# Optimization experiments

Hardware: AMD Instinct MI355X
Metric: run time of the kernel (lower is better)

Reference implementation:

```python
import jax, jax.numpy as jnp
import numpy as np

B, K, C, H, W = 16, 32, 256, 80, 80
NH, HD = 8, 32          # num_heads, head_dim (C = NH*HD)
S = 4                   # fixed roi_align sampling grid per 1x1 output bin
EPS = 1e-5


def _bn(x, g, b, m, v):
    # inference-mode BatchNorm2d, NCHW
    s = g / jnp.sqrt(v + EPS)
    return x * s[None, :, None, None] + (b - m * s)[None, :, None, None]


def _bilinear(feat, ys, xs):
    # feat [B,C,H,W]; ys,xs [B,K,S,S] -> [B,K,S,S,C], torchvision roi_align semantics
    Hh, Ww = feat.shape[2], feat.shape[3]
    valid = (ys >= -1.0) & (ys <= Hh) & (xs >= -1.0) & (xs <= Ww)
    y = jnp.clip(ys, 0.0, Hh - 1.0)
    x = jnp.clip(xs, 0.0, Ww - 1.0)
    y0 = jnp.floor(y); x0 = jnp.floor(x)
    y0i = y0.astype(jnp.int32); x0i = x0.astype(jnp.int32)
    y1i = jnp.minimum(y0i + 1, Hh - 1); x1i = jnp.minimum(x0i + 1, Ww - 1)
    ly = y - y0; lx = x - x0; hy = 1.0 - ly; hx = 1.0 - lx
    bidx = jnp.arange(feat.shape[0])[:, None, None, None]
    g = lambda yi, xi: feat[bidx, :, yi, xi]  # -> [B,K,S,S,C]
    val = ((hy * hx)[..., None] * g(y0i, x0i) + (hy * lx)[..., None] * g(y0i, x1i)
           + (ly * hx)[..., None] * g(y1i, x0i) + (ly * lx)[..., None] * g(y1i, x1i))
    return val * valid[..., None].astype(val.dtype)


def _roi_align_1x1(feat, boxes):
    # boxes [B,K,4] normalized xyxy; spatial_scale = 1.0 in the source
    Hh, Ww = feat.shape[2], feat.shape[3]
    sc = jnp.asarray([Ww - 1, Hh - 1, Ww - 1, Hh - 1], feat.dtype)
    ab = boxes * sc
    x1, y1, x2, y2 = ab[..., 0], ab[..., 1], ab[..., 2], ab[..., 3]
    rw = jnp.maximum(x2 - x1, 1.0)
    rh = jnp.maximum(y2 - y1, 1.0)
    grid = (jnp.arange(S, dtype=feat.dtype) + 0.5) / S
    ys = y1[..., None] + grid * rh[..., None]   # [B,K,S]
    xs = x1[..., None] + grid * rw[..., None]
    ys2, xs2 = jnp.broadcast_arrays(ys[..., :, None], xs[..., None, :])  # [B,K,S,S]
    vals = _bilinear(feat, ys2, xs2)            # [B,K,S,S,C]
    return vals.mean(axis=(2, 3)).reshape(feat.shape[0] * boxes.shape[1], -1)


def _gat(nodes, wq, bq, wk, bkp, wv, bv, scale, wo, bo, ln_g, ln_b):
    Bk = nodes.shape[0]
    q = (nodes @ wq.T + bq).reshape(Bk, NH, HD)
    k = (nodes @ wk.T + bkp).reshape(Bk, NH, HD)
    v = (nodes @ wv.T + bv).reshape(Bk, NH, HD)
    scores = jnp.einsum('ihd,jhd->ijh', q, k) * scale
    attn = jax.nn.softmax(scores, axis=1)       # softmax over keys j
    msg = jnp.einsum('ijh,jhd->ihd', attn, v).reshape(Bk, NH * HD)
    y = nodes + msg @ wo.T + bo
    mu = y.mean(-1, keepdims=True)
    var = ((y - mu) ** 2).mean(-1, keepdims=True)
    return (y - mu) / jnp.sqrt(var + EPS) * ln_g + ln_b


def _forward(x, boxes, conv_w, conv_b, bn1_g, bn1_b, bn1_m, bn1_v,
             wq, bq, wk, bkp, wv, bv, scale, wo, bo, ln_g, ln_b,
             rec_w, rec_b, bn2_g, bn2_b, bn2_m, bn2_v):
    feat = jax.lax.conv_general_dilated(
        x, conv_w, (1, 1), 'SAME',
        dimension_numbers=('NCHW', 'OIHW', 'NCHW')) + conv_b[None, :, None, None]
    feat = _bn(feat, bn1_g, bn1_b, bn1_m, bn1_v)
    feat = feat * jax.nn.sigmoid(feat)          # SiLU
    nodes = _roi_align_1x1(feat, boxes)         # [B*K, C]
    enh = _gat(nodes, wq, bq, wk, bkp, wv, bv, scale, wo, bo, ln_g, ln_b)
    f = enh.reshape(B, K, C)
    wts = jax.nn.softmax(f.mean(-1), axis=1)    # [B,K]
    weighted = jnp.einsum('bkc,bk->bc', f, wts)
    # out map is spatially constant -> 1x1 conv + BN collapse to per-sample affine
    y = weighted @ rec_w[:, :, 0, 0].T + rec_b
    s = bn2_g / jnp.sqrt(bn2_v + EPS)
    y = y * s + (bn2_b - bn2_m * s)
    return x + y[:, :, None, None]


def setup_inputs() -> dict:
    key = jax.random.key(0)
    ks = jax.random.split(key, 10)
    x = jax.random.normal(ks[0], (B, C, H, W), jnp.float32)
    bx = jax.random.uniform(ks[1], (B, K, 4), jnp.float32)
    bx = bx.at[:, :, 2:].add(bx[:, :, :2])      # xy2 += xy1
    boxes = jnp.clip(bx, 0.0, 1.0)
    w = lambda k, shp: jax.random.normal(k, shp, jnp.float32) * 0.02
    return {
        'x': x, 'boxes': boxes,
        'conv_w': w(ks[2], (C, C, 3, 3)), 'conv_b': jnp.zeros((C,), jnp.float32),
        'bn1_g': jnp.ones((C,), jnp.float32), 'bn1_b': jnp.zeros((C,), jnp.float32),
        'bn1_m': jnp.zeros((C,), jnp.float32), 'bn1_v': jnp.ones((C,), jnp.float32),
        'wq': w(ks[3], (C, C)), 'bq': jnp.zeros((C,), jnp.float32),
        'wk': w(ks[4], (C, C)), 'bkp': jnp.zeros((C,), jnp.float32),
        'wv': w(ks[5], (C, C)), 'bv': jnp.zeros((C,), jnp.float32),
        'scale': jnp.asarray(1.0 / np.sqrt(HD), jnp.float32),
        'wo': w(ks[6], (C, C)), 'bo': jnp.zeros((C,), jnp.float32),
        'ln_g': jnp.ones((C,), jnp.float32), 'ln_b': jnp.zeros((C,), jnp.float32),
        'rec_w': w(ks[7], (C, C, 1, 1)), 'rec_b': jnp.zeros((C,), jnp.float32),
        'bn2_g': jnp.ones((C,), jnp.float32), 'bn2_b': jnp.zeros((C,), jnp.float32),
        'bn2_m': jnp.zeros((C,), jnp.float32), 'bn2_v': jnp.ones((C,), jnp.float32),
    }


def reference(x, boxes, conv_w, conv_b, bn1_g, bn1_b, bn1_m, bn1_v,
              wq, bq, wk, bkp, wv, bv, scale, wo, bo, ln_g, ln_b,
              rec_w, rec_b, bn2_g, bn2_b, bn2_m, bn2_v):
    return _forward(x, boxes, conv_w, conv_b, bn1_g, bn1_b, bn1_m, bn1_v,
                    wq, bq, wk, bkp, wv, bv, scale, wo, bo, ln_g, ln_b,
                    rec_w, rec_b, bn2_g, bn2_b, bn2_m, bn2_v)
```

## Files before the change

### kernel.cpp

```cpp
#include <hip/hip_runtime.h>

#define EPSV 1e-5f

typedef __attribute__((ext_vector_type(8))) short short8v;
typedef __attribute__((ext_vector_type(4))) float f32x4;

static __device__ __forceinline__ unsigned short f2bf(float f) {
  unsigned int u = __float_as_uint(f);
  u += 0x7fff + ((u >> 16) & 1);
  return (unsigned short)(u >> 16);
}
static __device__ __forceinline__ float bf2f(unsigned short h) {
  return __uint_as_float(((unsigned int)h) << 16);
}

static __device__ __forceinline__ void glds16(const void* g, void* l) {
  __builtin_amdgcn_global_load_lds(
      (const __attribute__((address_space(1))) void*)g,
      (__attribute__((address_space(3))) void*)l, 16, 0, 0);
}

__global__ __launch_bounds__(256) void prep_fused_kernel(
    const float* __restrict__ x, unsigned short* __restrict__ xin,
    const float* __restrict__ cw, unsigned short* __restrict__ Wr,
    float* __restrict__ zpad,
    const float* __restrict__ wq, const float* __restrict__ wk,
    const float* __restrict__ wv, const float* __restrict__ wo,
    const float* __restrict__ rec, float* __restrict__ wT)
{
  __shared__ unsigned short t[80 * 257];
  const int bid = blockIdx.x;
  if (bid < 1280) {
    int b = bid / 80, y = bid - b * 80;
    const float* src = x + (size_t)b * 256 * 6400 + y * 80;
    for (int e = threadIdx.x; e < 256 * 20; e += 256) {
      int c = e / 20;
      int px4 = e - c * 20;
      f32x4 v = *(const f32x4*)&src[(size_t)c * 6400 + px4 * 4];
#pragma unroll
      for (int j = 0; j < 4; ++j)
        t[(px4 * 4 + j) * 257 + c] = f2bf(v[j]);
    }
    __syncthreads();
    unsigned short* dst = xin + (size_t)bid * 80 * 256;
    for (int e = threadIdx.x; e < 80 * 32; e += 256) {
      int px = e >> 5;
      int c8 = e & 31;
      short8v v;
#pragma unroll
      for (int j = 0; j < 8; ++j) v[j] = t[px * 257 + c8 * 8 + j];
      *(short8v*)&dst[px * 256 + c8 * 8] = v;
    }
  } else if (bid < 3584) {
    if (bid == 1280) zpad[threadIdx.x] = 0.f;
    int idx = (bid - 1280) * 256 + threadIdx.x;
    int cil = idx & 31;
    int rest = idx >> 5;
    int co = rest & 255;
    int tcc = rest >> 8;
    int cc = tcc & 7;
    int tt = tcc >> 3;
    int dy = tt / 3, dx = tt - dy * 3;
    int ci = cc * 32 + cil;
    Wr[idx] = f2bf(cw[((co * 256 + ci) * 3 + dy) * 3 + dx]);
  } else {
    int idx = (bid - 3584) * 256 + threadIdx.x;
    int m = idx >> 16;
    int e = idx & 65535;
    int ci = e >> 8, co = e & 255;
    const float* src = (m == 0) ? wq : (m == 1) ? wk : (m == 2) ? wv
                     : (m == 3) ? wo : rec;
    wT[idx] = src[co * 256 + ci];
  }
}

__global__ __launch_bounds__(512, 1) void roiconv_kernel(
    const unsigned short* __restrict__ xin,
    const float* __restrict__ boxes,
    const float* __restrict__ convb,
    const float* __restrict__ bn1g, const float* __restrict__ bn1b,
    const float* __restrict__ bn1m, const float* __restrict__ bn1v,
    const unsigned short* __restrict__ Wr,
    float* __restrict__ nodes)
{
  const int bid = blockIdx.x;
  const int pr = (bid & 7) * 32 + (bid >> 3);
  const int tid = threadIdx.x;
  const int nd = tid >> 8;
  const int n = pr * 2 + nd;
  const int b = n >> 5;
  const int w = tid >> 6, lane = tid & 63;
  const int bq = lane >> 4, r16 = lane & 15;
  const int wr = w >> 2, wc = w & 3;

  __shared__ __align__(16) char lds[74240];
  float* wcoef = (float*)(lds + 73728);
  const int INB = 0, WB = 24576;

  const int pc = (tid >> 2) & 63;
  const float* bx = boxes + n * 4;
  float x1 = bx[0] * 79.f, y1 = bx[1] * 79.f, x2 = bx[2] * 79.f, y2 = bx[3] * 79.f;
  float rwd = fmaxf(x2 - x1, 1.f), rh = fmaxf(y2 - y1, 1.f);
  int s = pc >> 2;
  int sy = s >> 2, sx = s & 3;
  float yy = y1 + (sy + 0.5f) * 0.25f * rh;
  float xx = x1 + (sx + 0.5f) * 0.25f * rwd;
  bool valid = (yy >= -1.f) && (yy <= 80.f) && (xx >= -1.f) && (xx <= 80.f);
  float yc = fminf(fmaxf(yy, 0.f), 79.f), xc = fminf(fmaxf(xx, 0.f), 79.f);
  float y0f = floorf(yc), x0f = floorf(xc);
  int y0i = (int)y0f, x0i = (int)x0f;
  int y1i = min(y0i + 1, 79), x1i = min(x0i + 1, 79);
  float ly = yc - y0f, lx = xc - x0f, hy = 1.f - ly, hx = 1.f - lx;
  int py = (pc & 2) ? y1i : y0i;
  int pxx = (pc & 1) ? x1i : x0i;
  if ((tid & 3) == 0)
    wcoef[tid >> 2] = ((pc & 2) ? ly : hy) * ((pc & 1) ? lx : hx) *
                      (valid ? 0.0625f : 0.f);

  const int chunk = (tid & 3) ^ ((pc >> 1) & 3);
  unsigned ioff[9];
#pragma unroll
  for (int t = 0; t < 9; ++t) {
    int dy = t / 3, dx = t - dy * 3;
    int cy = py + dy - 1, cx = pxx + dx - 1;
    bool ok = ((unsigned)cy < 80u) && ((unsigned)cx < 80u);
    ioff[t] = ok ? (unsigned)((((b * 80 + cy) * 80 + cx) * 256 + chunk * 8) * 2)
                 : 52428800u;
  }
  unsigned woff[2];
#pragma unroll
  for (int i = 0; i < 2; ++i) {
    int s2 = tid + (i << 9);
    int wco = s2 >> 2;
    int wch = (s2 & 3) ^ ((wco >> 1) & 3);
    woff[i] = (unsigned)((wco * 32 + wch * 8) * 2);
  }
  const int laneoff = r16 * 64 + ((bq ^ ((r16 >> 1) & 3)) << 4);
  const char* xinb = (const char*)xin;
  const char* Wrb = (const char*)Wr;
  const int ldwave = w << 10;

  f32x4 acc[4][4];
#pragma unroll
  for (int i = 0; i < 4; ++i)
#pragma unroll
    for (int j = 0; j < 4; ++j)
      acc[i][j] = (f32x4){0.f, 0.f, 0.f, 0.f};

  glds16(xinb + ioff[0], lds + INB + ldwave);
  glds16(Wrb + woff[0], lds + WB + ldwave);
  glds16(Wrb + woff[1], lds + WB + 8192 + ldwave);
  glds16(xinb + ioff[1], lds + INB + 8192 + ldwave);
  glds16(Wrb + ((size_t)8 << 14) + woff[0], lds + WB + 16384 + ldwave);
  glds16(Wrb + ((size_t)8 << 14) + woff[1], lds + WB + 16384 + 8192 + ldwave);

  for (int cc = 0; cc < 8; ++cc) {
#pragma unroll
    for (int t = 0; t < 9; ++t) {
      const int cb = t % 3;
      const char* inb = lds + INB + cb * 8192;
      const char* wb  = lds + WB + cb * 16384;
      if (cc == 7 && t == 8)
        asm volatile("s_waitcnt vmcnt(0)" ::: "memory");
      else
        asm volatile("s_waitcnt vmcnt(3)" ::: "memory");
      __builtin_amdgcn_s_barrier();
      __builtin_amdgcn_sched_barrier(0);
      if (!(cc == 7 && t >= 7)) {
        const int nt = (t + 2 > 8) ? t - 7 : t + 2;
        const int nb = nt % 3;
        const int ncc = cc + (t >= 7 ? 1 : 0);
        char* innx = lds + INB + nb * 8192;
        char* wbn  = lds + WB + nb * 16384;
        glds16(xinb + ioff[nt] + ncc * 64, innx + ldwave);
        const char* wg = Wrb + ((size_t)(nt * 8 + ncc) << 14);
        glds16(wg + woff[0], wbn + ldwave);
        glds16(wg + woff[1], wbn + 8192 + ldwave);
      }
      const char* pa = inb + wr * 4096 + laneoff;
      const char* pw = wb + wc * 4096 + laneoff;
      short8v af0 = *(const short8v*)(pa);
      short8v af1 = *(const short8v*)(pa + 1024);
      short8v af2 = *(const short8v*)(pa + 2048);
      short8v af3 = *(const short8v*)(pa + 3072);
      short8v wf0 = *(const short8v*)(pw);
      short8v wf1 = *(const short8v*)(pw + 1024);
      short8v wf2 = *(const short8v*)(pw + 2048);
      short8v wf3 = *(const short8v*)(pw + 3072);
      __builtin_amdgcn_s_setprio(1);
      acc[0][0] = __builtin_amdgcn_mfma_f32_16x16x32_bf16(af0, wf0, acc[0][0], 0, 0, 0);
      acc[0][1] = __builtin_amdgcn_mfma_f32_16x16x32_bf16(af0, wf1, acc[0][1], 0, 0, 0);
      acc[0][2] = __builtin_amdgcn_mfma_f32_16x16x32_bf16(af0, wf2, acc[0][2], 0, 0, 0);
      acc[0][3] = __builtin_amdgcn_mfma_f32_16x16x32_bf16(af0, wf3, acc[0][3], 0, 0, 0);
      acc[1][0] = __builtin_amdgcn_mfma_f32_16x16x32_bf16(af1, wf0, acc[1][0], 0, 0, 0);
      acc[1][1] = __builtin_amdgcn_mfma_f32_16x16x32_bf16(af1, wf1, acc[1][1], 0, 0, 0);
      acc[1][2] = __builtin_amdgcn_mfma_f32_16x16x32_bf16(af1, wf2, acc[1][2], 0, 0, 0);
      acc[1][3] = __builtin_amdgcn_mfma_f32_16x16x32_bf16(af1, wf3, acc[1][3], 0, 0, 0);
      acc[2][0] = __builtin_amdgcn_mfma_f32_16x16x32_bf16(af2, wf0, acc[2][0], 0, 0, 0);
      acc[2][1] = __builtin_amdgcn_mfma_f32_16x16x32_bf16(af2, wf1, acc[2][1], 0, 0, 0);
      acc[2][2] = __builtin_amdgcn_mfma_f32_16x16x32_bf16(af2, wf2, acc[2][2], 0, 0, 0);
      acc[2][3] = __builtin_amdgcn_mfma_f32_16x16x32_bf16(af2, wf3, acc[2][3], 0, 0, 0);
      acc[3][0] = __builtin_amdgcn_mfma_f32_16x16x32_bf16(af3, wf0, acc[3][0], 0, 0, 0);
      acc[3][1] = __builtin_amdgcn_mfma_f32_16x16x32_bf16(af3, wf1, acc[3][1], 0, 0, 0);
      acc[3][2] = __builtin_amdgcn_mfma_f32_16x16x32_bf16(af3, wf2, acc[3][2], 0, 0, 0);
      acc[3][3] = __builtin_amdgcn_mfma_f32_16x16x32_bf16(af3, wf3, acc[3][3], 0, 0, 0);
      __builtin_amdgcn_s_setprio(0);
    }
  }
  __syncthreads();

  unsigned short* ep = (unsigned short*)lds;
#pragma unroll
  for (int cf = 0; cf < 4; ++cf) {
    int co = wc * 64 + cf * 16 + r16;
    float sc = bn1g[co] / sqrtf(bn1v[co] + EPSV);
    float sh = bn1b[co] - bn1m[co] * sc;
    float cb = convb[co];
#pragma unroll
    for (int mf = 0; mf < 4; ++mf) {
#pragma unroll
      for (int rg = 0; rg < 4; ++rg) {
        int pxo = wr * 64 + mf * 16 + bq * 4 + rg;
        float v = (acc[mf][cf][rg] + cb) * sc + sh;
        v = v / (1.f + __expf(-v));
        ep[pxo * 264 + co] = f2bf(v);
      }
    }
  }
  __syncthreads();
  const int c = tid & 255;
  float val = 0.f;
#pragma unroll
  for (int p = 0; p < 64; ++p)
    val += wcoef[nd * 64 + p] * bf2f(ep[(nd * 64 + p) * 264 + c]);
  nodes[n * 256 + c] = val;
}

__global__ __launch_bounds__(256) void qkv_kernel(
    const float* __restrict__ nodes, const float* __restrict__ wT,
    const float* __restrict__ bq, const float* __restrict__ bk,
    const float* __restrict__ bv,
    float* __restrict__ q, float* __restrict__ k, float* __restrict__ v)
{
  const int blk = blockIdx.x;
  const int co = threadIdx.x;
  __shared__ float nd[4][256];
  for (int i = threadIdx.x; i < 1024; i += 256)
    nd[i >> 8][i & 255] = nodes[blk * 1024 + i];
  __syncthreads();
  float aq[4] = {0, 0, 0, 0};
  float ak[4] = {0, 0, 0, 0};
  float av[4] = {0, 0, 0, 0};
  const float* wqT = wT;
  const float* wkT = wT + 65536;
  const float* wvT = wT + 131072;
  for (int ci = 0; ci < 256; ++ci) {
    float wq_ = wqT[ci * 256 + co];
    float wk_ = wkT[ci * 256 + co];
    float wv_ = wvT[ci * 256 + co];
#pragma unroll
    for (int r = 0; r < 4; ++r) {
      float nv = nd[r][ci];
      aq[r] += nv * wq_;
      ak[r] += nv * wk_;
      av[r] += nv * wv_;
    }
  }
  float bq_ = bq[co], bk_ = bk[co], bv_ = bv[co];
#pragma unroll
  for (int r = 0; r < 4; ++r) {
    int n = blk * 4 + r;
    q[n * 256 + co] = aq[r] + bq_;
    k[n * 256 + co] = ak[r] + bk_;
    v[n * 256 + co] = av[r] + bv_;
  }
}

__global__ __launch_bounds__(256) void attn_mh_kernel(
    const float* __restrict__ q, const float* __restrict__ k,
    const float* __restrict__ v, const float* __restrict__ scale_p,
    float* __restrict__ msgs)
{
  const int bid = blockIdx.x;
  const int h = bid & 7, qc = bid >> 3;
  const int q0 = qc * 16;
  const int tid = threadIdx.x;
  __shared__ __align__(16) float Kh[512 * 32];
  __shared__ __align__(16) float Vh[512 * 32];
  __shared__ unsigned short pb[16 * 512];

  for (int idx = tid; idx < 4096; idx += 256) {
    int j = idx >> 3, part = idx & 7;
    int chs = part ^ (j & 7);
    *(f32x4*)&Kh[j * 32 + chs * 4] =
        *(const f32x4*)&k[(size_t)j * 256 + h * 32 + part * 4];
    *(f32x4*)&Vh[j * 32 + chs * 4] =
        *(const f32x4*)&v[(size_t)j * 256 + h * 32 + part * 4];
  }
  const int qi = tid >> 4, l = tid & 15;
  f32x4 qr[8];
#pragma unroll
  for (int p = 0; p < 8; ++p)
    qr[p] = *(const f32x4*)&q[(size_t)(q0 + qi) * 256 + h * 32 + p * 4];
  const float scale = scale_p[0];
  __syncthreads();

  float pj[32];
  float mx = -1e30f;
#pragma unroll
  for (int jj = 0; jj < 32; ++jj) {
    int j = jj * 16 + l;
    const float* kr = &Kh[j * 32];
    int sw = j & 7;
    float s = 0.f;
#pragma unroll
    for (int p = 0; p < 8; ++p) {
      f32x4 kv = *(const f32x4*)&kr[(p ^ sw) * 4];
      s += kv.x * qr[p].x + kv.y * qr[p].y + kv.z * qr[p].z + kv.w * qr[p].w;
    }
    s *= scale;
    pj[jj] = s;
    mx = fmaxf(mx, s);
  }
#pragma unroll
  for (int o = 1; o < 16; o <<= 1) mx = fmaxf(mx, __shfl_xor(mx, o, 16));
  float sum = 0.f;
#pragma unroll
  for (int jj = 0; jj < 32; ++jj) {
    float e = __expf(pj[jj] - mx);
    pj[jj] = e;
    sum += e;
  }
#pragma unroll
  for (int o = 1; o < 16; o <<= 1) sum += __shfl_xor(sum, o, 16);
  float inv = 1.f / sum;
#pragma unroll
  for (int jj = 0; jj < 32; ++jj)
    pb[qi * 512 + jj * 16 + l] = f2bf(pj[jj] * inv);
  __syncthreads();

  float m0 = 0.f, m1 = 0.f;
  const unsigned short* pq = &pb[qi * 512];
  for (int j = 0; j < 512; ++j) {
    float p = bf2f(pq[j]);
    int chs = (l >> 1) ^ (j & 7);
    const float* vr = &Vh[j * 32 + chs * 4 + ((2 * l) & 3)];
    m0 += p * vr[0];
    m1 += p * vr[1];
  }
  float* mo = &msgs[(size_t)(q0 + qi) * 256 + h * 32 + 2 * l];
  mo[0] = m0;
  mo[1] = m1;
}

__global__ __launch_bounds__(256) void outln_kernel(
    const float* __restrict__ msgs, const float* __restrict__ nodes,
    const float* __restrict__ woT, const float* __restrict__ bo,
    const float* __restrict__ lng, const float* __restrict__ lnb,
    float* __restrict__ enh)
{
  const int blk = blockIdx.x;
  const int co = threadIdx.x;
  __shared__ float ms[8][256];
  __shared__ float red1[8][4], red2[8][4];
  for (int i = co; i < 2048; i += 256)
    ms[i >> 8][i & 255] = msgs[blk * 2048 + i];
  __syncthreads();
  float yv[8];
  float bo_ = bo[co];
#pragma unroll
  for (int r = 0; r < 8; ++r)
    yv[r] = nodes[(size_t)(blk * 8 + r) * 256 + co] + bo_;
  for (int ci = 0; ci < 256; ++ci) {
    float w = woT[ci * 256 + co];
#pragma unroll
    for (int r = 0; r < 8; ++r) yv[r] += ms[r][ci] * w;
  }
  const int wv = co >> 6, lane = co & 63;
#pragma unroll
  for (int r = 0; r < 8; ++r) {
    float s1 = yv[r], s2 = yv[r] * yv[r];
#pragma unroll
    for (int o = 1; o < 64; o <<= 1) {
      s1 += __shfl_xor(s1, o);
      s2 += __shfl_xor(s2, o);
    }
    if (lane == 0) { red1[r][wv] = s1; red2[r][wv] = s2; }
  }
  __syncthreads();
  float lg = lng[co], lb = lnb[co];
#pragma unroll
  for (int r = 0; r < 8; ++r) {
    float S1 = red1[r][0] + red1[r][1] + red1[r][2] + red1[r][3];
    float S2 = red2[r][0] + red2[r][1] + red2[r][2] + red2[r][3];
    float mu = S1 * (1.f / 256.f);
    float var = S2 * (1.f / 256.f) - mu * mu;
    enh[(size_t)(blk * 8 + r) * 256 + co] =
        (yv[r] - mu) * rsqrtf(var + EPSV) * lg + lb;
  }
}

__global__ __launch_bounds__(256) void final_kernel(
    const float* __restrict__ enh, const float* __restrict__ recT,
    const float* __restrict__ recb,
    const float* __restrict__ bn2g, const float* __restrict__ bn2b,
    const float* __restrict__ bn2m, const float* __restrict__ bn2v,
    float* __restrict__ yfin)
{
  const int b = blockIdx.x;
  const int tid = threadIdx.x;
  const int wv = tid >> 6, l = tid & 63;
  __shared__ float rm[32], wts[32], wgt[256];
  for (int kk = wv; kk < 32; kk += 4) {
    const float* er = enh + (size_t)(b * 32 + kk) * 256;
    float s = er[l] + er[l + 64] + er[l + 128] + er[l + 192];
#pragma unroll
    for (int o = 1; o < 64; o <<= 1) s += __shfl_xor(s, o);
    if (l == 0) rm[kk] = s * (1.f / 256.f);
  }
  __syncthreads();
  if (tid < 32) {
    float m = rm[tid];
    float mx = m;
#pragma unroll
    for (int o = 1; o < 32; o <<= 1) mx = fmaxf(mx, __shfl_xor(mx, o, 32));
    float e = __expf(m - mx);
    float sm = e;
#pragma unroll
    for (int o = 1; o < 32; o <<= 1) sm += __shfl_xor(sm, o, 32);
    wts[tid] = e / sm;
  }
  __syncthreads();
  float wsum = 0.f;
  for (int kk = 0; kk < 32; ++kk)
    wsum += enh[(size_t)(b * 32 + kk) * 256 + tid] * wts[kk];
  wgt[tid] = wsum;
  __syncthreads();
  const int co = tid;
  float yv = recb[co];
  for (int ci = 0; ci < 256; ++ci)
    yv += wgt[ci] * recT[ci * 256 + co];
  float s = bn2g[co] / sqrtf(bn2v[co] + EPSV);
  yfin[b * 256 + co] = yv * s + (bn2b[co] - bn2m[co] * s);
}

__global__ __launch_bounds__(256) void add_kernel(
    const float* __restrict__ x, const float* __restrict__ yfin,
    float* __restrict__ out)
{
  const int bc = blockIdx.x;
  const float a = yfin[bc];
  const f32x4* xp = (const f32x4*)(x + (size_t)bc * 6400);
  f32x4* op = (f32x4*)(out + (size_t)bc * 6400);
  for (int i = threadIdx.x; i < 1600; i += 256) {
    f32x4 v = xp[i];
    v.x += a; v.y += a; v.z += a; v.w += a;
    op[i] = v;
  }
}

extern "C" void kernel_launch(void* const* d_in, const int* in_sizes, int n_in,
                              void* d_out, int out_size, void* d_ws, size_t ws_size,
                              hipStream_t stream)
{
  const float* x      = (const float*)d_in[0];
  const float* boxes  = (const float*)d_in[1];
  const float* conv_w = (const float*)d_in[2];
  const float* conv_b = (const float*)d_in[3];
  const float* bn1g   = (const float*)d_in[4];
  const float* bn1b   = (const float*)d_in[5];
  const float* bn1m   = (const float*)d_in[6];
  const float* bn1v   = (const float*)d_in[7];
  const float* wq     = (const float*)d_in[8];
  const float* bq     = (const float*)d_in[9];
  const float* wk     = (const float*)d_in[10];
  const float* bkp    = (const float*)d_in[11];
  const float* wv     = (const float*)d_in[12];
  const float* bv     = (const float*)d_in[13];
  const float* scale  = (const float*)d_in[14];
  const float* wo     = (const float*)d_in[15];
  const float* bo     = (const float*)d_in[16];
  const float* lng    = (const float*)d_in[17];
  const float* lnb    = (const float*)d_in[18];
  const float* rec_w  = (const float*)d_in[19];
  const float* rec_b  = (const float*)d_in[20];
  const float* bn2g   = (const float*)d_in[21];
  const float* bn2b   = (const float*)d_in[22];
  const float* bn2m   = (const float*)d_in[23];
  const float* bn2v   = (const float*)d_in[24];
  float* out = (float*)d_out;

  char* ws = (char*)d_ws;
  unsigned short* Wr = (unsigned short*)(ws);
  float* wT    = (float*)(ws + 53608448);
  float* nodes = (float*)(ws + 54919168);
  float* qb    = nodes + 131072;
  float* kb    = qb + 131072;
  float* vb    = kb + 131072;
  float* enh   = vb + 131072;
  float* yfin  = enh + 131072;
  float* msgs  = yfin + 4096;

  unsigned short* xin = (unsigned short*)d_out;
  float* zpad = (float*)((char*)d_out + 52428800);

  hipLaunchKernelGGL(prep_fused_kernel, dim3(4864), dim3(256), 0, stream,
                     x, xin, conv_w, Wr, zpad, wq, wk, wv, wo, rec_w, wT);
  hipLaunchKernelGGL(roiconv_kernel, dim3(256), dim3(512), 0, stream,
                     xin, boxes, conv_b, bn1g, bn1b, bn1m, bn1v, Wr, nodes);
  hipLaunchKernelGGL(qkv_kernel, dim3(128), dim3(256), 0, stream,
                     nodes, wT, bq, bkp, bv, qb, kb, vb);
  hipLaunchKernelGGL(attn_mh_kernel, dim3(256), dim3(256), 0, stream,
                     qb, kb, vb, scale, msgs);
  hipLaunchKernelGGL(outln_kernel, dim3(64), dim3(256), 0, stream,
                     msgs, nodes, wT + 3 * 65536, bo, lng, lnb, enh);
  hipLaunchKernelGGL(final_kernel, dim3(16), dim3(256), 0, stream,
                     enh, wT + 4 * 65536, rec_b, bn2g, bn2b, bn2m, bn2v, yfin);
  hipLaunchKernelGGL(add_kernel, dim3(4096), dim3(256), 0, stream, x, yfin, out);
}
```

Baseline: 182.2 us.

## Split roiconv output channels across blocks and add residual from bf16 NHWC copy

The ROI conv kernel moves from 256 blocks of 512 threads to 512 blocks of 256 threads. Each block now handles both nodes of a pair but only half of the 256 output channels. This halves LDS per block and allows two blocks per CU, at the cost of loading the gathered input twice. The final residual add now reads the bf16 NHWC copy of x held in workspace instead of the fp32 input, and transposes it through LDS back to NCHW. That halves the residual read traffic but adds bf16 rounding error to the output.

New measurement: 187.6 us. +2.9%, slower.

```diff
diff --git a/kernel.cpp b/kernel.cpp
--- a/kernel.cpp
+++ b/kernel.cpp
@@ -74,7 +74,7 @@
   }
 }
 
-__global__ __launch_bounds__(512, 1) void roiconv_kernel(
+__global__ __launch_bounds__(256, 2) void roiconv_kernel(
     const unsigned short* __restrict__ xin,
     const float* __restrict__ boxes,
     const float* __restrict__ convb,
@@ -84,61 +84,65 @@
     float* __restrict__ nodes)
 {
   const int bid = blockIdx.x;
-  const int pr = (bid & 7) * 32 + (bid >> 3);
+  const int blk = (bid & 7) * 64 + (bid >> 3);
+  const int pr = blk >> 1, coh = blk & 1;
   const int tid = threadIdx.x;
-  const int nd = tid >> 8;
-  const int n = pr * 2 + nd;
-  const int b = n >> 5;
   const int w = tid >> 6, lane = tid & 63;
   const int bq = lane >> 4, r16 = lane & 15;
-  const int wr = w >> 2, wc = w & 3;
-
-  __shared__ __align__(16) char lds[74240];
-  float* wcoef = (float*)(lds + 73728);
+  const int wr = w >> 1, wc = w & 1;
+
+  __shared__ __align__(16) char lds[49664];
+  float* wcoef = (float*)(lds + 49152);
   const int INB = 0, WB = 24576;
 
-  const int pc = (tid >> 2) & 63;
-  const float* bx = boxes + n * 4;
-  float x1 = bx[0] * 79.f, y1 = bx[1] * 79.f, x2 = bx[2] * 79.f, y2 = bx[3] * 79.f;
-  float rwd = fmaxf(x2 - x1, 1.f), rh = fmaxf(y2 - y1, 1.f);
-  int s = pc >> 2;
-  int sy = s >> 2, sx = s & 3;
-  float yy = y1 + (sy + 0.5f) * 0.25f * rh;
-  float xx = x1 + (sx + 0.5f) * 0.25f * rwd;
-  bool valid = (yy >= -1.f) && (yy <= 80.f) && (xx >= -1.f) && (xx <= 80.f);
-  float yc = fminf(fmaxf(yy, 0.f), 79.f), xc = fminf(fmaxf(xx, 0.f), 79.f);
-  float y0f = floorf(yc), x0f = floorf(xc);
-  int y0i = (int)y0f, x0i = (int)x0f;
-  int y1i = min(y0i + 1, 79), x1i = min(x0i + 1, 79);
-  float ly = yc - y0f, lx = xc - x0f, hy = 1.f - ly, hx = 1.f - lx;
-  int py = (pc & 2) ? y1i : y0i;
-  int pxx = (pc & 1) ? x1i : x0i;
-  if ((tid & 3) == 0)
-    wcoef[tid >> 2] = ((pc & 2) ? ly : hy) * ((pc & 1) ? lx : hx) *
-                      (valid ? 0.0625f : 0.f);
-
-  const int chunk = (tid & 3) ^ ((pc >> 1) & 3);
-  unsigned ioff[9];
-#pragma unroll
-  for (int t = 0; t < 9; ++t) {
-    int dy = t / 3, dx = t - dy * 3;
-    int cy = py + dy - 1, cx = pxx + dx - 1;
-    bool ok = ((unsigned)cy < 80u) && ((unsigned)cx < 80u);
-    ioff[t] = ok ? (unsigned)((((b * 80 + cy) * 80 + cx) * 256 + chunk * 8) * 2)
-                 : 52428800u;
-  }
-  unsigned woff[2];
-#pragma unroll
-  for (int i = 0; i < 2; ++i) {
-    int s2 = tid + (i << 9);
-    int wco = s2 >> 2;
-    int wch = (s2 & 3) ^ ((wco >> 1) & 3);
-    woff[i] = (unsigned)((wco * 32 + wch * 8) * 2);
-  }
+  const int pc = tid >> 2;
+  const int swz = tid & 3;
+  const int chunk = swz ^ ((pc >> 1) & 3);
+  unsigned ioff[2][9];
+#pragma unroll
+  for (int nd2 = 0; nd2 < 2; ++nd2) {
+    const int n2 = pr * 2 + nd2;
+    const int b2 = n2 >> 5;
+    const float* bx = boxes + n2 * 4;
+    float x1 = bx[0] * 79.f, y1 = bx[1] * 79.f;
+    float x2 = bx[2] * 79.f, y2 = bx[3] * 79.f;
+    float rwd = fmaxf(x2 - x1, 1.f), rh = fmaxf(y2 - y1, 1.f);
+    int s = pc >> 2;
+    int sy = s >> 2, sx = s & 3;
+    float yy = y1 + (sy + 0.5f) * 0.25f * rh;
+    float xx = x1 + (sx + 0.5f) * 0.25f * rwd;
+    bool valid = (yy >= -1.f) && (yy <= 80.f) && (xx >= -1.f) && (xx <= 80.f);
+    float yc = fminf(fmaxf(yy, 0.f), 79.f), xc = fminf(fmaxf(xx, 0.f), 79.f);
+    float y0f = floorf(yc), x0f = floorf(xc);
+    int y0i = (int)y0f, x0i = (int)x0f;
+    int y1i = min(y0i + 1, 79), x1i = min(x0i + 1, 79);
+    float ly = yc - y0f, lx = xc - x0f, hy = 1.f - ly, hx = 1.f - lx;
+    int py = (pc & 2) ? y1i : y0i;
+    int pxx = (pc & 1) ? x1i : x0i;
+    if (swz == 0)
+      wcoef[nd2 * 64 + pc] = ((pc & 2) ? ly : hy) * ((pc & 1) ? lx : hx) *
+                             (valid ? 0.0625f : 0.f);
+#pragma unroll
+    for (int t = 0; t < 9; ++t) {
+      int dy = t / 3, dx = t - dy * 3;
+      int cy = py + dy - 1, cx = pxx + dx - 1;
+      bool ok = ((unsigned)cy < 80u) && ((unsigned)cx < 80u);
+      ioff[nd2][t] = ok
+          ? (unsigned)((((b2 * 80 + cy) * 80 + cx) * 256 + chunk * 8) * 2)
+          : 52428800u;
+    }
+  }
+  const int wco0 = tid >> 2;
+  const unsigned woff0 =
+      (unsigned)(coh * 8192 + (wco0 * 32 + ((swz ^ ((wco0 >> 1) & 3)) * 8)) * 2);
+  const int wco1 = 64 + wco0;
+  const unsigned woff1 =
+      (unsigned)(coh * 8192 + (wco1 * 32 + ((swz ^ ((wco1 >> 1) & 3)) * 8)) * 2);
+
   const int laneoff = r16 * 64 + ((bq ^ ((r16 >> 1) & 3)) << 4);
   const char* xinb = (const char*)xin;
   const char* Wrb = (const char*)Wr;
-  const int ldwave = w << 10;
+  const int ldwave = (w << 6) << 4;
 
   f32x4 acc[4][4];
 #pragma unroll
@@ -147,23 +151,25 @@
     for (int j = 0; j < 4; ++j)
       acc[i][j] = (f32x4){0.f, 0.f, 0.f, 0.f};
 
-  glds16(xinb + ioff[0], lds + INB + ldwave);
-  glds16(Wrb + woff[0], lds + WB + ldwave);
-  glds16(Wrb + woff[1], lds + WB + 8192 + ldwave);
-  glds16(xinb + ioff[1], lds + INB + 8192 + ldwave);
-  glds16(Wrb + ((size_t)8 << 14) + woff[0], lds + WB + 16384 + ldwave);
-  glds16(Wrb + ((size_t)8 << 14) + woff[1], lds + WB + 16384 + 8192 + ldwave);
+  glds16(xinb + ioff[0][0], lds + INB + ldwave);
+  glds16(xinb + ioff[1][0], lds + INB + 4096 + ldwave);
+  glds16(Wrb + woff0, lds + WB + ldwave);
+  glds16(Wrb + woff1, lds + WB + 4096 + ldwave);
+  glds16(xinb + ioff[0][1], lds + INB + 8192 + ldwave);
+  glds16(xinb + ioff[1][1], lds + INB + 8192 + 4096 + ldwave);
+  glds16(Wrb + ((size_t)8 << 14) + woff0, lds + WB + 8192 + ldwave);
+  glds16(Wrb + ((size_t)8 << 14) + woff1, lds + WB + 8192 + 4096 + ldwave);
 
   for (int cc = 0; cc < 8; ++cc) {
 #pragma unroll
     for (int t = 0; t < 9; ++t) {
       const int cb = t % 3;
       const char* inb = lds + INB + cb * 8192;
-      const char* wb  = lds + WB + cb * 16384;
+      const char* wb  = lds + WB + cb * 8192;
       if (cc == 7 && t == 8)
         asm volatile("s_waitcnt vmcnt(0)" ::: "memory");
       else
-        asm volatile("s_waitcnt vmcnt(3)" ::: "memory");
+        asm volatile("s_waitcnt vmcnt(4)" ::: "memory");
       __builtin_amdgcn_s_barrier();
       __builtin_amdgcn_sched_barrier(0);
       if (!(cc == 7 && t >= 7)) {
@@ -171,11 +177,12 @@
         const int nb = nt % 3;
         const int ncc = cc + (t >= 7 ? 1 : 0);
         char* innx = lds + INB + nb * 8192;
-        char* wbn  = lds + WB + nb * 16384;
-        glds16(xinb + ioff[nt] + ncc * 64, innx + ldwave);
+        char* wbn  = lds + WB + nb * 8192;
+        glds16(xinb + ioff[0][nt] + ncc * 64, innx + ldwave);
+        glds16(xinb + ioff[1][nt] + ncc * 64, innx + 4096 + ldwave);
         const char* wg = Wrb + ((size_t)(nt * 8 + ncc) << 14);
-        glds16(wg + woff[0], wbn + ldwave);
-        glds16(wg + woff[1], wbn + 8192 + ldwave);
+        glds16(wg + woff0, wbn + ldwave);
+        glds16(wg + woff1, wbn + 4096 + ldwave);
       }
       const char* pa = inb + wr * 4096 + laneoff;
       const char* pw = wb + wc * 4096 + laneoff;
@@ -212,10 +219,11 @@
   unsigned short* ep = (unsigned short*)lds;
 #pragma unroll
   for (int cf = 0; cf < 4; ++cf) {
-    int co = wc * 64 + cf * 16 + r16;
-    float sc = bn1g[co] / sqrtf(bn1v[co] + EPSV);
-    float sh = bn1b[co] - bn1m[co] * sc;
-    float cb = convb[co];
+    int col = wc * 64 + cf * 16 + r16;
+    int cog = coh * 128 + col;
+    float sc = bn1g[cog] / sqrtf(bn1v[cog] + EPSV);
+    float sh = bn1b[cog] - bn1m[cog] * sc;
+    float cb = convb[cog];
 #pragma unroll
     for (int mf = 0; mf < 4; ++mf) {
 #pragma unroll
@@ -223,17 +231,17 @@
         int pxo = wr * 64 + mf * 16 + bq * 4 + rg;
         float v = (acc[mf][cf][rg] + cb) * sc + sh;
         v = v / (1.f + __expf(-v));
-        ep[pxo * 264 + co] = f2bf(v);
+        ep[pxo * 136 + col] = f2bf(v);
       }
     }
   }
   __syncthreads();
-  const int c = tid & 255;
+  const int nd = tid >> 7, c = tid & 127;
   float val = 0.f;
 #pragma unroll
   for (int p = 0; p < 64; ++p)
-    val += wcoef[nd * 64 + p] * bf2f(ep[(nd * 64 + p) * 264 + c]);
-  nodes[n * 256 + c] = val;
+    val += wcoef[nd * 64 + p] * bf2f(ep[(nd * 64 + p) * 136 + c]);
+  nodes[(pr * 2 + nd) * 256 + coh * 128 + c] = val;
 }
 
 __global__ __launch_bounds__(256) void qkv_kernel(
@@ -444,18 +452,31 @@
   yfin[b * 256 + co] = yv * s + (bn2b[co] - bn2m[co] * s);
 }
 
-__global__ __launch_bounds__(256) void add_kernel(
-    const float* __restrict__ x, const float* __restrict__ yfin,
+__global__ __launch_bounds__(320) void add_kernel(
+    const unsigned short* __restrict__ xin, const float* __restrict__ yfin,
     float* __restrict__ out)
 {
-  const int bc = blockIdx.x;
-  const float a = yfin[bc];
-  const f32x4* xp = (const f32x4*)(x + (size_t)bc * 6400);
-  f32x4* op = (f32x4*)(out + (size_t)bc * 6400);
-  for (int i = threadIdx.x; i < 1600; i += 256) {
-    f32x4 v = xp[i];
-    v.x += a; v.y += a; v.z += a; v.w += a;
-    op[i] = v;
+  const int bid = blockIdx.x;
+  const int b = bid / 80, y = bid - b * 80;
+  const int tid = threadIdx.x;
+  __shared__ unsigned short ep[80 * 258];
+  __shared__ float yf[256];
+  const unsigned short* src = xin + (size_t)bid * 80 * 256;
+  for (int idx = tid; idx < 2560; idx += 320) {
+    int px = idx >> 5;
+    int c8 = idx & 31;
+    short8v v = *(const short8v*)&src[px * 256 + c8 * 8];
+    *(short8v*)&ep[px * 258 + c8 * 8] = v;
+  }
+  if (tid < 256) yf[tid] = yfin[b * 256 + tid];
+  __syncthreads();
+  const int cq = tid / 80;
+  const int px = tid - cq * 80;
+  float* ob = out + (size_t)b * 256 * 6400 + y * 80 + px;
+#pragma unroll 4
+  for (int k = 0; k < 64; ++k) {
+    int c = cq * 64 + k;
+    ob[(size_t)c * 6400] = bf2f(ep[px * 258 + c]) + yf[c];
   }
 }
 
@@ -492,21 +513,20 @@
 
   char* ws = (char*)d_ws;
   unsigned short* Wr = (unsigned short*)(ws);
-  float* wT    = (float*)(ws + 53608448);
-  float* nodes = (float*)(ws + 54919168);
+  float* wT    = (float*)(ws + 2097152);
+  float* nodes = (float*)(ws + 4194304);
   float* qb    = nodes + 131072;
   float* kb    = qb + 131072;
   float* vb    = kb + 131072;
   float* enh   = vb + 131072;
   float* yfin  = enh + 131072;
   float* msgs  = yfin + 4096;
-
-  unsigned short* xin = (unsigned short*)d_out;
-  float* zpad = (float*)((char*)d_out + 52428800);
+  unsigned short* xin = (unsigned short*)(ws + 8388608);
+  float* zpad = (float*)(ws + 8388608 + 52428800);
 
   hipLaunchKernelGGL(prep_fused_kernel, dim3(4864), dim3(256), 0, stream,
                      x, xin, conv_w, Wr, zpad, wq, wk, wv, wo, rec_w, wT);
-  hipLaunchKernelGGL(roiconv_kernel, dim3(256), dim3(512), 0, stream,
+  hipLaunchKernelGGL(roiconv_kernel, dim3(512), dim3(256), 0, stream,
                      xin, boxes, conv_b, bn1g, bn1b, bn1m, bn1v, Wr, nodes);
   hipLaunchKernelGGL(qkv_kernel, dim3(128), dim3(256), 0, stream,
                      nodes, wT, bq, bkp, bv, qb, kb, vb);
@@ -516,5 +536,6 @@
                      msgs, nodes, wT + 3 * 65536, bo, lng, lnb, enh);
   hipLaunchKernelGGL(final_kernel, dim3(16), dim3(256), 0, stream,
                      enh, wT + 4 * 65536, rec_b, bn2g, bn2b, bn2m, bn2v, yfin);
-  hipLaunchKernelGGL(add_kernel, dim3(4096), dim3(256), 0, stream, x, yfin, out);
-}
+  hipLaunchKernelGGL(add_kernel, dim3(1280), dim3(320), 0, stream,
+                     xin, yfin, out);
+}
```

## Build residual output from bf16 channels-last copy and split QKV grid

Applied to the files above, without the earlier changes.

The final add kernel now reads the bf16 channels-last copy of x, which was already built for the conv, instead of re-reading the fp32 input. It transposes each image row through LDS back to NCHW and adds the per-channel bias. That copy and its padding move from the output buffer into the workspace so the output can be written directly. The aim is to halve the read traffic of the bandwidth-bound final pass, but the residual term is now bf16-rounded, which loses precision on the output. Separately, the QKV projection is split across twice as many blocks, each handling half the output channels and half the rows, to raise parallelism.

Result: slower. 189.4 us (+3.9%).

```diff
diff --git a/kernel.cpp b/kernel.cpp
--- a/kernel.cpp
+++ b/kernel.cpp
@@ -243,14 +243,15 @@
     float* __restrict__ q, float* __restrict__ k, float* __restrict__ v)
 {
   const int blk = blockIdx.x;
-  const int co = threadIdx.x;
+  const int nq = blk >> 1, coh = blk & 1;
+  const int t = threadIdx.x;
+  const int co = coh * 128 + (t & 127);
+  const int half = t >> 7;
   __shared__ float nd[4][256];
-  for (int i = threadIdx.x; i < 1024; i += 256)
-    nd[i >> 8][i & 255] = nodes[blk * 1024 + i];
-  __syncthreads();
-  float aq[4] = {0, 0, 0, 0};
-  float ak[4] = {0, 0, 0, 0};
-  float av[4] = {0, 0, 0, 0};
+  for (int i = t; i < 1024; i += 256)
+    nd[i >> 8][i & 255] = nodes[nq * 1024 + i];
+  __syncthreads();
+  float aq[2] = {0, 0}, ak[2] = {0, 0}, av[2] = {0, 0};
   const float* wqT = wT;
   const float* wkT = wT + 65536;
   const float* wvT = wT + 131072;
@@ -259,8 +260,8 @@
     float wk_ = wkT[ci * 256 + co];
     float wv_ = wvT[ci * 256 + co];
 #pragma unroll
-    for (int r = 0; r < 4; ++r) {
-      float nv = nd[r][ci];
+    for (int r = 0; r < 2; ++r) {
+      float nv = nd[half * 2 + r][ci];
       aq[r] += nv * wq_;
       ak[r] += nv * wk_;
       av[r] += nv * wv_;
@@ -268,8 +269,8 @@
   }
   float bq_ = bq[co], bk_ = bk[co], bv_ = bv[co];
 #pragma unroll
-  for (int r = 0; r < 4; ++r) {
-    int n = blk * 4 + r;
+  for (int r = 0; r < 2; ++r) {
+    int n = nq * 4 + half * 2 + r;
     q[n * 256 + co] = aq[r] + bq_;
     k[n * 256 + co] = ak[r] + bk_;
     v[n * 256 + co] = av[r] + bv_;
@@ -445,17 +446,34 @@
 }
 
 __global__ __launch_bounds__(256) void add_kernel(
-    const float* __restrict__ x, const float* __restrict__ yfin,
+    const unsigned short* __restrict__ xin, const float* __restrict__ yfin,
     float* __restrict__ out)
 {
-  const int bc = blockIdx.x;
-  const float a = yfin[bc];
-  const f32x4* xp = (const f32x4*)(x + (size_t)bc * 6400);
-  f32x4* op = (f32x4*)(out + (size_t)bc * 6400);
-  for (int i = threadIdx.x; i < 1600; i += 256) {
-    f32x4 v = xp[i];
-    v.x += a; v.y += a; v.z += a; v.w += a;
-    op[i] = v;
+  const int bid = blockIdx.x;
+  const int b = bid / 80, y = bid - b * 80;
+  const int tid = threadIdx.x;
+  __shared__ unsigned short ep[80 * 258];
+  __shared__ float yf[256];
+  const unsigned short* src = xin + (size_t)bid * 80 * 256;
+  for (int idx = tid; idx < 2560; idx += 256) {
+    int px = idx >> 5;
+    int c8 = idx & 31;
+    *(short8v*)&ep[px * 258 + c8 * 8] = *(const short8v*)&src[px * 256 + c8 * 8];
+  }
+  yf[tid] = yfin[b * 256 + tid];
+  __syncthreads();
+  float* ob = out + (size_t)b * 256 * 6400 + y * 80;
+#pragma unroll
+  for (int k2 = 0; k2 < 20; ++k2) {
+    int idx = k2 * 256 + tid;
+    int c = idx / 20;
+    int px4 = idx - c * 20;
+    float a = yf[c];
+    f32x4 v;
+#pragma unroll
+    for (int j = 0; j < 4; ++j)
+      v[j] = bf2f(ep[(px4 * 4 + j) * 258 + c]) + a;
+    *(f32x4*)&ob[(size_t)c * 6400 + px4 * 4] = v;
   }
 }
 
@@ -492,23 +510,22 @@
 
   char* ws = (char*)d_ws;
   unsigned short* Wr = (unsigned short*)(ws);
-  float* wT    = (float*)(ws + 53608448);
-  float* nodes = (float*)(ws + 54919168);
+  float* wT    = (float*)(ws + 2097152);
+  float* nodes = (float*)(ws + 4194304);
   float* qb    = nodes + 131072;
   float* kb    = qb + 131072;
   float* vb    = kb + 131072;
   float* enh   = vb + 131072;
   float* yfin  = enh + 131072;
   float* msgs  = yfin + 4096;
-
-  unsigned short* xin = (unsigned short*)d_out;
-  float* zpad = (float*)((char*)d_out + 52428800);
+  unsigned short* xin = (unsigned short*)(ws + 8388608);
+  float* zpad = (float*)(ws + 8388608 + 52428800);
 
   hipLaunchKernelGGL(prep_fused_kernel, dim3(4864), dim3(256), 0, stream,
                      x, xin, conv_w, Wr, zpad, wq, wk, wv, wo, rec_w, wT);
   hipLaunchKernelGGL(roiconv_kernel, dim3(256), dim3(512), 0, stream,
                      xin, boxes, conv_b, bn1g, bn1b, bn1m, bn1v, Wr, nodes);
-  hipLaunchKernelGGL(qkv_kernel, dim3(128), dim3(256), 0, stream,
+  hipLaunchKernelGGL(qkv_kernel, dim3(256), dim3(256), 0, stream,
                      nodes, wT, bq, bkp, bv, qb, kb, vb);
   hipLaunchKernelGGL(attn_mh_kernel, dim3(256), dim3(256), 0, stream,
                      qb, kb, vb, scale, msgs);
@@ -516,5 +533,6 @@
                      msgs, nodes, wT + 3 * 65536, bo, lng, lnb, enh);
   hipLaunchKernelGGL(final_kernel, dim3(16), dim3(256), 0, stream,
                      enh, wT + 4 * 65536, rec_b, bn2g, bn2b, bn2m, bn2v, yfin);
-  hipLaunchKernelGGL(add_kernel, dim3(4096), dim3(256), 0, stream, x, yfin, out);
-}
+  hipLaunchKernelGGL(add_kernel, dim3(1280), dim3(256), 0, stream,
+                     xin, yfin, out);
+}
```
